# Kernel optimization log

Hardware: AMD Instinct MI355X
Metric: run time of the kernel (lower is better)

Reference implementation:

```python
import math
import jax, jax.numpy as jnp
import numpy as np

B, S, D, H = 2, 2048, 2048, 16  # batch, seq, d_model, n_heads


def setup_inputs() -> dict:
    key = jax.random.key(0)
    ks = jax.random.split(key, 5)
    w_scale = 1.0 / math.sqrt(D)
    return {
        "x": jax.random.normal(ks[0], (B, S, D), jnp.float32),
        "attn_bias": jax.random.normal(ks[1], (1, H, S, S), jnp.float32) * 0.1,
        "Wqkv_w": jax.random.normal(ks[2], (3 * D, D), jnp.float32) * w_scale,
        "Wqkv_b": jnp.zeros((3 * D,), jnp.float32),
        "out_w": jax.random.normal(ks[3], (D, D), jnp.float32) * w_scale,
        "out_b": jnp.zeros((D,), jnp.float32),
    }


def reference(x, attn_bias, Wqkv_w, Wqkv_b, out_w, out_b):
    b, s, d = x.shape
    hd = d // H                      # head dim = 128
    scale = 1.0 / math.sqrt(hd)      # module default: 1/sqrt(d_model // n_heads)

    # fused QKV projection
    qkv = x @ Wqkv_w.T + Wqkv_b                       # [b, s, 3d]
    q, k, v = jnp.split(qkv, 3, axis=2)               # each [b, s, d]
    q = q.reshape(b, s, H, hd).transpose(0, 2, 1, 3)  # [b, h, s, hd]
    k = k.reshape(b, s, H, hd).transpose(0, 2, 1, 3)
    v = v.reshape(b, s, H, hd).transpose(0, 2, 1, 3)

    # scaled scores + additive bias (bias sliced to trailing q/k lengths)
    scores = jnp.einsum('bhqd,bhkd->bhqk', q, k) * scale
    scores = scores + attn_bias[:, :, -s:, -s:]

    # causal mask, masked positions set to dtype min (matches masked_fill with finfo.min)
    causal = jnp.tril(jnp.ones((s, s), dtype=bool))   # True = keep
    min_val = jnp.finfo(scores.dtype).min
    scores = jnp.where(causal[None, None, :, :], scores, min_val)

    p = jax.nn.softmax(scores, axis=-1)               # [b, h, s, s]
    out = jnp.einsum('bhqk,bhkd->bhqd', p, v)         # [b, h, s, hd]
    out = out.transpose(0, 2, 1, 3).reshape(b, s, d)  # [b, s, d]

    return out @ out_w.T + out_b
```

## Files before the change

kernel.cpp:

```cpp
#include <hip/hip_runtime.h>
#include <hip/hip_bf16.h>
#include <stdint.h>

#define H_  16
#define S_  2048
#define D_  2048
#define HD_ 128

typedef __bf16 bf16x8 __attribute__((ext_vector_type(8)));
typedef short  s16x8  __attribute__((ext_vector_type(8)));
typedef float  f32x4  __attribute__((ext_vector_type(4)));
typedef unsigned short u16x4 __attribute__((ext_vector_type(4)));

__device__ __forceinline__ unsigned short f2bf(float f) {
    unsigned u = __builtin_bit_cast(unsigned, f);
    u += 0x7fffu + ((u >> 16) & 1u);
    return (unsigned short)(u >> 16);
}

__device__ __forceinline__ bf16x8 ld_bf8(const unsigned short* p) {
    s16x8 r = *reinterpret_cast<const s16x8*>(p);
    return __builtin_bit_cast(bf16x8, r);
}

#define GLOAD_LDS16(gp, lp)                                                     \
    __builtin_amdgcn_global_load_lds(                                            \
        (const __attribute__((address_space(1))) void*)(gp),                     \
        (__attribute__((address_space(3))) void*)(lp), 16, 0, 0)

__global__ __launch_bounds__(256) void cast_f32_bf16(const float* __restrict__ in,
                                                     unsigned short* __restrict__ out,
                                                     int n) {
    int i = (blockIdx.x * 256 + threadIdx.x) * 4;
    if (i >= n) return;
    float4 v = *reinterpret_cast<const float4*>(in + i);
    u16x4 o;
    o[0] = f2bf(v.x); o[1] = f2bf(v.y); o[2] = f2bf(v.z); o[3] = f2bf(v.w);
    *reinterpret_cast<u16x4*>(out + i) = o;
}

__device__ __forceinline__ void gemm128_core(const unsigned short* __restrict__ Aptr,
                                             const unsigned short* __restrict__ Bptr,
                                             int m0, int n0,
                                             unsigned short* As, unsigned short* Bs,
                                             f32x4 acc[4][4]) {
    const int t  = threadIdx.x;
    const int l  = t & 63, w = t >> 6;
    const int wr = w >> 1, wc = w & 1;
    const int lr = l & 15, g = l >> 4;

    f32x4 zero = {0.f, 0.f, 0.f, 0.f};
#pragma unroll
    for (int i = 0; i < 4; ++i)
#pragma unroll
        for (int j = 0; j < 4; ++j) acc[i][j] = zero;

    for (int kt = 0; kt < D_; kt += 64) {
#pragma unroll
        for (int p = 0; p < 4; ++p) {
            int lin = (p * 256 + t) * 16;
            int row = lin >> 7, colb = lin & 127;
            int scol = (colb ^ ((row & 7) << 4)) >> 1;
            GLOAD_LDS16(Aptr + (size_t)(m0 + row) * D_ + kt + scol, &As[lin >> 1]);
        }
#pragma unroll
        for (int p = 0; p < 4; ++p) {
            int lin = (p * 256 + t) * 16;
            int row = lin >> 7, colb = lin & 127;
            int scol = (colb ^ ((row & 7) << 4)) >> 1;
            GLOAD_LDS16(Bptr + (size_t)(n0 + row) * D_ + kt + scol, &Bs[lin >> 1]);
        }
        __syncthreads();
#pragma unroll
        for (int ks = 0; ks < 2; ++ks) {
            bf16x8 af[4], bfr[4];
#pragma unroll
            for (int mi = 0; mi < 4; ++mi)
                af[mi] = ld_bf8(&As[(wr * 64 + mi * 16 + lr) * 64 +
                                    ((ks * 32 + g * 8) ^ ((lr & 7) << 3))]);
#pragma unroll
            for (int ni = 0; ni < 4; ++ni)
                bfr[ni] = ld_bf8(&Bs[(wc * 64 + ni * 16 + lr) * 64 +
                                     ((ks * 32 + g * 8) ^ ((lr & 7) << 3))]);
#pragma unroll
            for (int mi = 0; mi < 4; ++mi)
#pragma unroll
                for (int ni = 0; ni < 4; ++ni)
                    acc[mi][ni] = __builtin_amdgcn_mfma_f32_16x16x32_bf16(
                        af[mi], bfr[ni], acc[mi][ni], 0, 0, 0);
        }
        __syncthreads();
    }
}

__global__ __launch_bounds__(256) void gemm_bt_qkv(const unsigned short* __restrict__ A,
                                                   const unsigned short* __restrict__ W,
                                                   const float* __restrict__ bias,
                                                   unsigned short* __restrict__ Qo,
                                                   unsigned short* __restrict__ Ko,
                                                   unsigned short* __restrict__ Vo) {
    __shared__ alignas(16) unsigned short As[128 * 64];
    __shared__ alignas(16) unsigned short Bs[128 * 64];

    const int GX = 48, NWG = 1536, CPX = NWG / 8;
    const int raw = blockIdx.y * GX + blockIdx.x;
    const int swz = (raw & 7) * CPX + (raw >> 3);
    const int m0 = (swz / GX) * 128, n0 = (swz % GX) * 128;

    f32x4 acc[4][4];
    gemm128_core(A, W, m0, n0, As, Bs, acc);

    const int l  = threadIdx.x & 63, w = threadIdx.x >> 6;
    const int wr = w >> 1, wc = w & 1;
    const int lr = l & 15, g = l >> 4;

    const int which = n0 >> 11;
    const int h     = (n0 & 2047) >> 7;
    const int b     = m0 >> 11;
    const int sb    = m0 & 2047;

    float bias_v[4];
#pragma unroll
    for (int ni = 0; ni < 4; ++ni)
        bias_v[ni] = bias[n0 + wc * 64 + ni * 16 + lr];

    if (which == 2) {
        unsigned short* Vb = Vo + ((size_t)(b * H_ + h)) * HD_ * S_;
#pragma unroll
        for (int mi = 0; mi < 4; ++mi) {
#pragma unroll
            for (int ni = 0; ni < 4; ++ni) {
                int d = wc * 64 + ni * 16 + lr;
                int s = sb + wr * 64 + mi * 16 + g * 4;
                u16x4 pv;
#pragma unroll
                for (int i = 0; i < 4; ++i) pv[i] = f2bf(acc[mi][ni][i] + bias_v[ni]);
                *reinterpret_cast<u16x4*>(&Vb[(size_t)d * S_ + s]) = pv;
            }
        }
    } else {
        unsigned short* Pb = ((which == 0) ? Qo : Ko) + ((size_t)(b * H_ + h)) * S_ * HD_;
#pragma unroll
        for (int mi = 0; mi < 4; ++mi) {
#pragma unroll
            for (int ni = 0; ni < 4; ++ni) {
                int d = wc * 64 + ni * 16 + lr;
#pragma unroll
                for (int i = 0; i < 4; ++i) {
                    int s = sb + wr * 64 + mi * 16 + g * 4 + i;
                    Pb[(size_t)s * HD_ + d] = f2bf(acc[mi][ni][i] + bias_v[ni]);
                }
            }
        }
    }
}

__global__ __launch_bounds__(256) void gemm_bt_out(const unsigned short* __restrict__ A,
                                                   const unsigned short* __restrict__ W,
                                                   const float* __restrict__ bias,
                                                   float* __restrict__ out) {
    __shared__ alignas(16) unsigned short As[128 * 64];
    __shared__ alignas(16) unsigned short Bs[128 * 64];

    const int GX = 16, NWG = 512, CPX = NWG / 8;
    const int raw = blockIdx.y * GX + blockIdx.x;
    const int swz = (raw & 7) * CPX + (raw >> 3);
    const int m0 = (swz / GX) * 128, n0 = (swz % GX) * 128;

    f32x4 acc[4][4];
    gemm128_core(A, W, m0, n0, As, Bs, acc);

    const int l  = threadIdx.x & 63, w = threadIdx.x >> 6;
    const int wr = w >> 1, wc = w & 1;
    const int lr = l & 15, g = l >> 4;

    for (int mi = 0; mi < 4; ++mi) {
        for (int ni = 0; ni < 4; ++ni) {
            for (int i = 0; i < 4; ++i) {
                int m = m0 + wr * 64 + mi * 16 + g * 4 + i;
                int n = n0 + wc * 64 + ni * 16 + lr;
                out[(size_t)m * D_ + n] = acc[mi][ni][i] + bias[n];
            }
        }
    }
}

__global__ __launch_bounds__(256) void attn_kernel10(const unsigned short* __restrict__ Q,
                                                     const unsigned short* __restrict__ K,
                                                     const unsigned short* __restrict__ Vt,
                                                     const float* __restrict__ biasPtr,
                                                     unsigned short* __restrict__ O) {
    __shared__ alignas(16) unsigned short Klds[2][4096];
    __shared__ alignas(16) unsigned short Vlds[2][4096];
    __shared__ alignas(16) unsigned short Pbuf[4][16 * 32];

    const int t  = threadIdx.x;
    const int l  = t & 63, w = t >> 6;
    const int lr = l & 15, g = l >> 4;

    const int raw   = blockIdx.x;
    const int xcd   = raw & 7;
    const int local = raw >> 3;
    const int cu    = local & 31;
    const int slot  = local >> 5;
    const int qt    = (slot & 1) ? cu : (31 - cu);
    const int bh    = xcd + 8 * slot;
    const int b     = bh >> 4, head = bh & 15;

    const unsigned short* Qb = Q + (size_t)bh * S_ * HD_;
    const unsigned short* Kb = K + (size_t)bh * S_ * HD_;
    const unsigned short* Vb = Vt + (size_t)bh * HD_ * S_;
    const float* Bh32 = biasPtr + (size_t)head * S_ * S_;
    const float scale = 0.08838834764831845f;

    const int q0 = qt * 64 + w * 16;

    bf16x8 qf[4];
#pragma unroll
    for (int dc = 0; dc < 4; ++dc)
        qf[dc] = ld_bf8(Qb + (size_t)(q0 + lr) * HD_ + dc * 32 + g * 8);

    f32x4 zero = {0.f, 0.f, 0.f, 0.f};
    f32x4 o[8];
#pragma unroll
    for (int nc = 0; nc < 8; ++nc) o[nc] = zero;
    float lp[4] = {0.f, 0.f, 0.f, 0.f};

    unsigned short* Pw = Pbuf[w];

    auto STAGE = [&](int buf, int k0) {
#pragma unroll
        for (int p = 0; p < 2; ++p) {
            int lin = p * 4096 + t * 16;
            int row = lin >> 8;
            int colb = lin & 255;
            int scolb = colb ^ ((row & 7) << 4);
            GLOAD_LDS16(Kb + (size_t)(k0 + row) * HD_ + (scolb >> 1), &Klds[buf][lin >> 1]);
        }
#pragma unroll
        for (int p = 0; p < 2; ++p) {
            int lin = p * 4096 + t * 16;
            int row = lin >> 6;
            int colb = lin & 63;
            int scolb = colb ^ ((row & 3) << 4);
            GLOAD_LDS16(Vb + (size_t)row * S_ + k0 + (scolb >> 1), &Vlds[buf][lin >> 1]);
        }
    };

    STAGE(0, 0);
    __syncthreads();

    const int nch = 2 * qt + 2;
    int cur = 0;
    for (int c = 0; c < nch; ++c) {
        const int k0 = c * 32;

        if (c + 1 < nch) STAGE(cur ^ 1, k0 + 32);

        float bias_r[4][2];
#pragma unroll
        for (int i = 0; i < 4; ++i) {
            const int boff = (q0 + g * 4 + i) * S_ + k0 + lr;
#pragma unroll
            for (int kc = 0; kc < 2; ++kc)
                bias_r[i][kc] = Bh32[boff + kc * 16];
        }

        f32x4 s[2];
        s[0] = zero; s[1] = zero;
#pragma unroll
        for (int kc = 0; kc < 2; ++kc) {
            bf16x8 kf[4];
#pragma unroll
            for (int dc = 0; dc < 4; ++dc)
                kf[dc] = ld_bf8(&Klds[cur][(kc * 16 + lr) * 128 + ((dc * 32 + g * 8) ^ ((lr & 7) << 3))]);
#pragma unroll
            for (int dc = 0; dc < 4; ++dc)
                s[kc] = __builtin_amdgcn_mfma_f32_16x16x32_bf16(qf[dc], kf[dc], s[kc], 0, 0, 0);
        }

        const bool maskzone = (c >= nch - 2);
#pragma unroll
        for (int i = 0; i < 4; ++i) {
            const int rowabs = q0 + g * 4 + i;
            const int prow   = g * 4 + i;
            float e[2];
#pragma unroll
            for (int kc = 0; kc < 2; ++kc) {
                float v = s[kc][i] * scale + bias_r[i][kc];
                if (maskzone && (k0 + kc * 16 + lr > rowabs)) v = -1.0e30f;
                e[kc] = __expf(v - 16.0f);
            }
            lp[i] += e[0] + e[1];
            const int sw = (prow & 3) << 3;
            Pw[(prow * 32 + 0  + lr) ^ sw] = f2bf(e[0]);
            Pw[(prow * 32 + 16 + lr) ^ sw] = f2bf(e[1]);
        }

        {
            bf16x8 pa = ld_bf8(&Pw[lr * 32 + ((g * 8) ^ ((lr & 3) << 3))]);
#pragma unroll
            for (int nc = 0; nc < 8; ++nc) {
                bf16x8 vf = ld_bf8(&Vlds[cur][(nc * 16 + lr) * 32 + ((g * 8) ^ ((lr & 3) << 3))]);
                o[nc] = __builtin_amdgcn_mfma_f32_16x16x32_bf16(pa, vf, o[nc], 0, 0, 0);
            }
        }

        __syncthreads();
        cur ^= 1;
    }

#pragma unroll
    for (int i = 0; i < 4; ++i) {
        lp[i] += __shfl_xor(lp[i], 1);
        lp[i] += __shfl_xor(lp[i], 2);
        lp[i] += __shfl_xor(lp[i], 4);
        lp[i] += __shfl_xor(lp[i], 8);
    }

#pragma unroll
    for (int i = 0; i < 4; ++i) {
        float inv = 1.0f / lp[i];
        int row = q0 + g * 4 + i;
#pragma unroll
        for (int nc = 0; nc < 8; ++nc) {
            O[((size_t)(b * S_ + row)) * D_ + head * HD_ + nc * 16 + lr] = f2bf(o[nc][i] * inv);
        }
    }
}

extern "C" void kernel_launch(void* const* d_in, const int* in_sizes, int n_in,
                              void* d_out, int out_size, void* d_ws, size_t ws_size,
                              hipStream_t stream) {
    (void)in_sizes; (void)n_in; (void)out_size; (void)ws_size;
    const float* x         = (const float*)d_in[0];
    const float* attn_bias = (const float*)d_in[1];
    const float* Wqkv_w    = (const float*)d_in[2];
    const float* Wqkv_b    = (const float*)d_in[3];
    const float* out_w     = (const float*)d_in[4];
    const float* out_b     = (const float*)d_in[5];
    float* out = (float*)d_out;

    char* ws = (char*)d_ws;
    unsigned short* xb    = (unsigned short*)(ws);
    unsigned short* wqkvb = (unsigned short*)(ws + 16777216);
    unsigned short* woutb = (unsigned short*)(ws + 41943040);
    unsigned short* Qb    = (unsigned short*)(ws + 50331648);
    unsigned short* Kb    = (unsigned short*)(ws + 67108864);
    unsigned short* Vtb   = (unsigned short*)(ws + 83886080);
    unsigned short* Ob    = xb;

    cast_f32_bf16<<<8192, 256, 0, stream>>>(x, xb, 8388608);
    cast_f32_bf16<<<12288, 256, 0, stream>>>(Wqkv_w, wqkvb, 12582912);
    cast_f32_bf16<<<4096, 256, 0, stream>>>(out_w, woutb, 4194304);
    gemm_bt_qkv<<<dim3(48, 32), 256, 0, stream>>>(xb, wqkvb, Wqkv_b, Qb, Kb, Vtb);
    attn_kernel10<<<1024, 256, 0, stream>>>(Qb, Kb, Vtb, attn_bias, Ob);
    gemm_bt_out<<<dim3(16, 32), 256, 0, stream>>>(Ob, woutb, out_b, out);
}
```

Before: 310.1 us.

## Triple-buffer K/V tiles in attention and fuse three cast kernels

The attention kernel now keeps three LDS stages for K and V instead of two. It prefetches two chunks ahead, and the full __syncthreads at the end of each iteration becomes a vmcnt wait plus a raw s_barrier, so global loads have more time to complete behind compute. The three fp32-to-bf16 cast launches are merged into one grid that picks its source and destination by block index, removing two launches. LDS use rises by about 16KB per block, which could lower occupancy. The hand-written vmcnt counts must also match the outstanding loads exactly, including the bias loads issued between stages.

```diff
diff --git a/kernel.cpp b/kernel.cpp
--- a/kernel.cpp
+++ b/kernel.cpp
@@ -28,11 +28,20 @@
         (const __attribute__((address_space(1))) void*)(gp),                     \
         (__attribute__((address_space(3))) void*)(lp), 16, 0, 0)
 
-__global__ __launch_bounds__(256) void cast_f32_bf16(const float* __restrict__ in,
-                                                     unsigned short* __restrict__ out,
-                                                     int n) {
-    int i = (blockIdx.x * 256 + threadIdx.x) * 4;
-    if (i >= n) return;
+__global__ __launch_bounds__(256) void cast3_f32_bf16(const float* __restrict__ i0,
+                                                      unsigned short* __restrict__ o0,
+                                                      const float* __restrict__ i1,
+                                                      unsigned short* __restrict__ o1,
+                                                      const float* __restrict__ i2,
+                                                      unsigned short* __restrict__ o2) {
+    const int bid = blockIdx.x;
+    const float* in;
+    unsigned short* out;
+    int base;
+    if (bid < 8192)       { in = i0; out = o0; base = bid; }
+    else if (bid < 20480) { in = i1; out = o1; base = bid - 8192; }
+    else                  { in = i2; out = o2; base = bid - 20480; }
+    int i = (base * 256 + threadIdx.x) * 4;
     float4 v = *reinterpret_cast<const float4*>(in + i);
     u16x4 o;
     o[0] = f2bf(v.x); o[1] = f2bf(v.y); o[2] = f2bf(v.z); o[3] = f2bf(v.w);
@@ -185,13 +194,13 @@
     }
 }
 
-__global__ __launch_bounds__(256) void attn_kernel10(const unsigned short* __restrict__ Q,
+__global__ __launch_bounds__(256) void attn_kernel11(const unsigned short* __restrict__ Q,
                                                      const unsigned short* __restrict__ K,
                                                      const unsigned short* __restrict__ Vt,
                                                      const float* __restrict__ biasPtr,
                                                      unsigned short* __restrict__ O) {
-    __shared__ alignas(16) unsigned short Klds[2][4096];
-    __shared__ alignas(16) unsigned short Vlds[2][4096];
+    __shared__ alignas(16) unsigned short Klds[3][4096];
+    __shared__ alignas(16) unsigned short Vlds[3][4096];
     __shared__ alignas(16) unsigned short Pbuf[4][16 * 32];
 
     const int t  = threadIdx.x;
@@ -247,16 +256,17 @@
         }
     };
 
+    const int nch = 2 * qt + 2;
+
     STAGE(0, 0);
-    __syncthreads();
-
-    const int nch = 2 * qt + 2;
+    STAGE(1, 32);
+    asm volatile("s_waitcnt vmcnt(4)" ::: "memory");
+    __builtin_amdgcn_s_barrier();
+
     int cur = 0;
     for (int c = 0; c < nch; ++c) {
         const int k0 = c * 32;
 
-        if (c + 1 < nch) STAGE(cur ^ 1, k0 + 32);
-
         float bias_r[4][2];
 #pragma unroll
         for (int i = 0; i < 4; ++i) {
@@ -265,6 +275,9 @@
             for (int kc = 0; kc < 2; ++kc)
                 bias_r[i][kc] = Bh32[boff + kc * 16];
         }
+
+        int s2 = cur + 2; if (s2 >= 3) s2 -= 3;
+        if (c + 2 < nch) STAGE(s2, k0 + 64);
 
         f32x4 s[2];
         s[0] = zero; s[1] = zero;
@@ -306,8 +319,12 @@
             }
         }
 
-        __syncthreads();
-        cur ^= 1;
+        if (c + 1 < nch) {
+            if (c + 2 < nch) { asm volatile("s_waitcnt vmcnt(4)" ::: "memory"); }
+            else             { asm volatile("s_waitcnt vmcnt(0)" ::: "memory"); }
+            __builtin_amdgcn_s_barrier();
+        }
+        cur = (cur == 2) ? 0 : cur + 1;
     }
 
 #pragma unroll
@@ -350,10 +367,8 @@
     unsigned short* Vtb   = (unsigned short*)(ws + 83886080);
     unsigned short* Ob    = xb;
 
-    cast_f32_bf16<<<8192, 256, 0, stream>>>(x, xb, 8388608);
-    cast_f32_bf16<<<12288, 256, 0, stream>>>(Wqkv_w, wqkvb, 12582912);
-    cast_f32_bf16<<<4096, 256, 0, stream>>>(out_w, woutb, 4194304);
+    cast3_f32_bf16<<<24576, 256, 0, stream>>>(x, xb, Wqkv_w, wqkvb, out_w, woutb);
     gemm_bt_qkv<<<dim3(48, 32), 256, 0, stream>>>(xb, wqkvb, Wqkv_b, Qb, Kb, Vtb);
-    attn_kernel10<<<1024, 256, 0, stream>>>(Qb, Kb, Vtb, attn_bias, Ob);
+    attn_kernel11<<<1024, 256, 0, stream>>>(Qb, Kb, Vtb, attn_bias, Ob);
     gemm_bt_out<<<dim3(16, 32), 256, 0, stream>>>(Ob, woutb, out_b, out);
 }
```

New measurement: 328.4 us. 5.9% more time.

## Replace QKV GEMM with 256x256 double-buffered 8-wave kernel with interleaved staging

Applied to the files above, without the earlier changes.

Swaps the 128x128 single-buffered QKV projection GEMM for a 256x256-tile kernel that runs 8 waves and double-buffers LDS. Global-to-LDS loads for the next K slice are split into quarters and interleaved with MFMA work, with barrier and priority hints. The larger tile raises operand reuse and cuts global traffic, and the overlap hides load latency. In exchange it needs 128KB of LDS, which limits occupancy to one block per CU, and the grid shrinks to 384 blocks, which may leave some CUs with uneven load.

```diff
diff --git a/kernel.cpp b/kernel.cpp
--- a/kernel.cpp
+++ b/kernel.cpp
@@ -39,6 +39,168 @@
     *reinterpret_cast<u16x4*>(out + i) = o;
 }
 
+__global__ __launch_bounds__(512) void gemm8_qkv(const unsigned short* __restrict__ Aptr,
+                                                 const unsigned short* __restrict__ Bptr,
+                                                 const float* __restrict__ bias,
+                                                 unsigned short* __restrict__ Qo,
+                                                 unsigned short* __restrict__ Ko,
+                                                 unsigned short* __restrict__ Vo) {
+    __shared__ alignas(16) unsigned short Ab[2][256 * 64];
+    __shared__ alignas(16) unsigned short Bb[2][256 * 64];
+
+    const int t  = threadIdx.x;
+    const int l  = t & 63, w = t >> 6;
+    const int wm = w >> 2, wn = w & 3;
+    const int lr = l & 15, g = l >> 4;
+
+    const int raw = blockIdx.x;
+    const int swz = (raw & 7) * 48 + (raw >> 3);
+    const int m0 = (swz / 24) * 256, n0 = (swz % 24) * 256;
+
+    f32x4 zero = {0.f, 0.f, 0.f, 0.f};
+    f32x4 acc[8][4];
+#pragma unroll
+    for (int i = 0; i < 8; ++i)
+#pragma unroll
+        for (int j = 0; j < 4; ++j) acc[i][j] = zero;
+
+    auto STAGE_A = [&](int buf, int kt, int half) {
+#pragma unroll
+        for (int p2 = 0; p2 < 2; ++p2) {
+            int lin = (p2 * 512 + t) * 16;
+            int row = (lin >> 7) + half * 128;
+            int colb = lin & 127;
+            int scol = (colb ^ ((row & 7) << 4)) >> 1;
+            GLOAD_LDS16(Aptr + (size_t)(m0 + row) * D_ + kt + scol,
+                        &Ab[buf][half * 128 * 64 + (lin >> 1)]);
+        }
+    };
+    auto STAGE_B = [&](int buf, int kt, int half) {
+#pragma unroll
+        for (int p2 = 0; p2 < 2; ++p2) {
+            int lin = (p2 * 512 + t) * 16;
+            int row = (lin >> 7) + half * 128;
+            int colb = lin & 127;
+            int scol = (colb ^ ((row & 7) << 4)) >> 1;
+            GLOAD_LDS16(Bptr + (size_t)(n0 + row) * D_ + kt + scol,
+                        &Bb[buf][half * 128 * 64 + (lin >> 1)]);
+        }
+    };
+
+    STAGE_A(0, 0, 0); STAGE_A(0, 0, 1);
+    STAGE_B(0, 0, 0); STAGE_B(0, 0, 1);
+    asm volatile("s_waitcnt vmcnt(0)" ::: "memory");
+    __builtin_amdgcn_s_barrier();
+
+    bf16x8 bfr[4][2];
+
+    const int NIT = 16;
+    for (int it = 0; it < NIT; ++it) {
+#pragma unroll
+        for (int half2 = 0; half2 < 2; ++half2) {
+            const int cb   = half2;
+            const int ct   = 2 * it + half2;
+            const int ckt  = ct * 64;
+            const int st   = 2 * it + 1 + half2;
+            const int skt  = st * 64;
+            const int sb   = cb ^ 1;
+            const bool doStage = (st < 32);
+
+#pragma unroll
+            for (int q = 0; q < 4; ++q) {
+                bf16x8 af[2][2];
+#pragma unroll
+                for (int s2 = 0; s2 < 2; ++s2)
+#pragma unroll
+                    for (int ks = 0; ks < 2; ++ks)
+                        af[s2][ks] = ld_bf8(&Ab[cb][(wm * 128 + q * 32 + s2 * 16 + lr) * 64 +
+                                                    ((ks * 32 + g * 8) ^ ((lr & 7) << 3))]);
+                if (q == 0) {
+#pragma unroll
+                    for (int ni = 0; ni < 4; ++ni)
+#pragma unroll
+                        for (int ks = 0; ks < 2; ++ks)
+                            bfr[ni][ks] = ld_bf8(&Bb[cb][(wn * 64 + ni * 16 + lr) * 64 +
+                                                         ((ks * 32 + g * 8) ^ ((lr & 7) << 3))]);
+                }
+
+                if (doStage) {
+                    if (q == 0)      STAGE_A(sb, skt, 0);
+                    else if (q == 1) STAGE_A(sb, skt, 1);
+                    else if (q == 2) STAGE_B(sb, skt, 0);
+                    else             STAGE_B(sb, skt, 1);
+                }
+
+                __builtin_amdgcn_s_barrier();
+                asm volatile("s_waitcnt lgkmcnt(0)" ::: "memory");
+                __builtin_amdgcn_sched_barrier(0);
+
+                __builtin_amdgcn_s_setprio(1);
+#pragma unroll
+                for (int ks = 0; ks < 2; ++ks)
+#pragma unroll
+                    for (int s2 = 0; s2 < 2; ++s2)
+#pragma unroll
+                        for (int ni = 0; ni < 4; ++ni)
+                            acc[q * 2 + s2][ni] = __builtin_amdgcn_mfma_f32_16x16x32_bf16(
+                                af[s2][ks], bfr[ni][ks], acc[q * 2 + s2][ni], 0, 0, 0);
+                __builtin_amdgcn_s_setprio(0);
+
+                if (q == 3) {
+                    asm volatile("s_waitcnt vmcnt(0)" ::: "memory");
+                }
+                __builtin_amdgcn_s_barrier();
+            }
+        }
+    }
+
+    const int which = n0 >> 11;
+    const int b     = m0 >> 11;
+    const int sb_   = m0 & 2047;
+
+    float bias_v[4];
+    int   h_v[4];
+#pragma unroll
+    for (int ni = 0; ni < 4; ++ni) {
+        int n = n0 + wn * 64 + ni * 16 + lr;
+        bias_v[ni] = bias[n];
+        h_v[ni]    = (n & 2047) >> 7;
+    }
+
+    if (which == 2) {
+#pragma unroll
+        for (int mi = 0; mi < 8; ++mi) {
+#pragma unroll
+            for (int ni = 0; ni < 4; ++ni) {
+                int n = n0 + wn * 64 + ni * 16 + lr;
+                int d = n & 127;
+                int s = sb_ + wm * 128 + mi * 16 + g * 4;
+                unsigned short* Vb = Vo + ((size_t)(b * H_ + h_v[ni])) * HD_ * S_;
+                u16x4 pv;
+#pragma unroll
+                for (int i = 0; i < 4; ++i) pv[i] = f2bf(acc[mi][ni][i] + bias_v[ni]);
+                *reinterpret_cast<u16x4*>(&Vb[(size_t)d * S_ + s]) = pv;
+            }
+        }
+    } else {
+        unsigned short* Base = (which == 0) ? Qo : Ko;
+#pragma unroll
+        for (int mi = 0; mi < 8; ++mi) {
+#pragma unroll
+            for (int ni = 0; ni < 4; ++ni) {
+                int n = n0 + wn * 64 + ni * 16 + lr;
+                int d = n & 127;
+                unsigned short* Pb = Base + ((size_t)(b * H_ + h_v[ni])) * S_ * HD_;
+#pragma unroll
+                for (int i = 0; i < 4; ++i) {
+                    int s = sb_ + wm * 128 + mi * 16 + g * 4 + i;
+                    Pb[(size_t)s * HD_ + d] = f2bf(acc[mi][ni][i] + bias_v[ni]);
+                }
+            }
+        }
+    }
+}
+
 __device__ __forceinline__ void gemm128_core(const unsigned short* __restrict__ Aptr,
                                              const unsigned short* __restrict__ Bptr,
                                              int m0, int n0,
@@ -90,68 +252,6 @@
                         af[mi], bfr[ni], acc[mi][ni], 0, 0, 0);
         }
         __syncthreads();
-    }
-}
-
-__global__ __launch_bounds__(256) void gemm_bt_qkv(const unsigned short* __restrict__ A,
-                                                   const unsigned short* __restrict__ W,
-                                                   const float* __restrict__ bias,
-                                                   unsigned short* __restrict__ Qo,
-                                                   unsigned short* __restrict__ Ko,
-                                                   unsigned short* __restrict__ Vo) {
-    __shared__ alignas(16) unsigned short As[128 * 64];
-    __shared__ alignas(16) unsigned short Bs[128 * 64];
-
-    const int GX = 48, NWG = 1536, CPX = NWG / 8;
-    const int raw = blockIdx.y * GX + blockIdx.x;
-    const int swz = (raw & 7) * CPX + (raw >> 3);
-    const int m0 = (swz / GX) * 128, n0 = (swz % GX) * 128;
-
-    f32x4 acc[4][4];
-    gemm128_core(A, W, m0, n0, As, Bs, acc);
-
-    const int l  = threadIdx.x & 63, w = threadIdx.x >> 6;
-    const int wr = w >> 1, wc = w & 1;
-    const int lr = l & 15, g = l >> 4;
-
-    const int which = n0 >> 11;
-    const int h     = (n0 & 2047) >> 7;
-    const int b     = m0 >> 11;
-    const int sb    = m0 & 2047;
-
-    float bias_v[4];
-#pragma unroll
-    for (int ni = 0; ni < 4; ++ni)
-        bias_v[ni] = bias[n0 + wc * 64 + ni * 16 + lr];
-
-    if (which == 2) {
-        unsigned short* Vb = Vo + ((size_t)(b * H_ + h)) * HD_ * S_;
-#pragma unroll
-        for (int mi = 0; mi < 4; ++mi) {
-#pragma unroll
-            for (int ni = 0; ni < 4; ++ni) {
-                int d = wc * 64 + ni * 16 + lr;
-                int s = sb + wr * 64 + mi * 16 + g * 4;
-                u16x4 pv;
-#pragma unroll
-                for (int i = 0; i < 4; ++i) pv[i] = f2bf(acc[mi][ni][i] + bias_v[ni]);
-                *reinterpret_cast<u16x4*>(&Vb[(size_t)d * S_ + s]) = pv;
-            }
-        }
-    } else {
-        unsigned short* Pb = ((which == 0) ? Qo : Ko) + ((size_t)(b * H_ + h)) * S_ * HD_;
-#pragma unroll
-        for (int mi = 0; mi < 4; ++mi) {
-#pragma unroll
-            for (int ni = 0; ni < 4; ++ni) {
-                int d = wc * 64 + ni * 16 + lr;
-#pragma unroll
-                for (int i = 0; i < 4; ++i) {
-                    int s = sb + wr * 64 + mi * 16 + g * 4 + i;
-                    Pb[(size_t)s * HD_ + d] = f2bf(acc[mi][ni][i] + bias_v[ni]);
-                }
-            }
-        }
     }
 }
 
@@ -353,7 +453,7 @@
     cast_f32_bf16<<<8192, 256, 0, stream>>>(x, xb, 8388608);
     cast_f32_bf16<<<12288, 256, 0, stream>>>(Wqkv_w, wqkvb, 12582912);
     cast_f32_bf16<<<4096, 256, 0, stream>>>(out_w, woutb, 4194304);
-    gemm_bt_qkv<<<dim3(48, 32), 256, 0, stream>>>(xb, wqkvb, Wqkv_b, Qb, Kb, Vtb);
+    gemm8_qkv<<<384, 512, 0, stream>>>(xb, wqkvb, Wqkv_b, Qb, Kb, Vtb);
     attn_kernel10<<<1024, 256, 0, stream>>>(Qb, Kb, Vtb, attn_bias, Ob);
     gemm_bt_out<<<dim3(16, 32), 256, 0, stream>>>(Ob, woutb, out_b, out);
 }
```

New measurement: 305.5 us. No clear change (-1.5%).
